# Kernel tuning notes

Measured on AMD Instinct MI355X. Metric: run time of the kernel, lower is better.

## Reference

```python
import jax, jax.numpy as jnp
import numpy as np

EPS = 1e-7  # same clamp torch BCE effectively applies to avoid log(0)


def _level_bce(att, boxes, valid, area, level_id, H, W):
    # att: [B, h_l, w_l] predicted attention in (0,1); boxes: [B, N, 4]; valid/area: [B, N]
    B, hl, wl = att.shape
    base = 2.0 ** (level_id + 5)
    min_area = base * base * 0.5
    max_area = (base * 1.58) ** 2 * 2.0
    sel = valid & (area >= min_area) & (area <= max_area)  # [B, N]
    sx = wl / W
    sy = hl / H
    # rasterization bounds on the level grid (int() == floor for non-negative coords)
    x1 = jnp.maximum(jnp.floor(boxes[..., 0] * sx), 0.0)
    y1 = jnp.maximum(jnp.floor(boxes[..., 1] * sy), 0.0)
    x2 = jnp.minimum(jnp.ceil(boxes[..., 2] * sx) + 1.0, float(wl))
    y2 = jnp.minimum(jnp.ceil(boxes[..., 3] * sy) + 1.0, float(hl))
    rows = jnp.arange(hl, dtype=att.dtype)
    cols = jnp.arange(wl, dtype=att.dtype)
    # separable per-box row/col indicators -> matmul-style OR to avoid a [B,N,h,w] tensor
    rin = (sel[..., None] & (rows >= y1[..., None]) & (rows < y2[..., None])).astype(att.dtype)  # [B,N,h]
    cin = (sel[..., None] & (cols >= x1[..., None]) & (cols < x2[..., None])).astype(att.dtype)  # [B,N,w]
    mask_gt = (jnp.einsum('bnh,bnw->bhw', rin, cin) > 0).astype(att.dtype)  # [B,h,w]
    p = jnp.clip(att, EPS, 1.0 - EPS)
    bce = -(mask_gt * jnp.log(p) + (1.0 - mask_gt) * jnp.log1p(-p))
    return bce.mean(axis=(1, 2))  # [B]


def reference(att0, att1, att2, att3, att4, bboxs, h, w):
    atts = [att0, att1, att2, att3, att4]
    hf = float(h)
    wf = float(w)
    x1, y1, x2, y2, label = (bboxs[..., i] for i in range(5))
    valid = (label != -1) & (x1 <= wf) & (y1 <= hf) & (x2 <= wf) & (y2 <= hf)  # [B,N]
    area = (x2 - x1) * (y2 - y1)
    boxes = bboxs[..., :4]
    per_level = [
        _level_bce(a[:, 0, :, :], boxes, valid, area, i, hf, wf)
        for i, a in enumerate(atts)
    ]
    sample_loss = jnp.stack(per_level, axis=0).mean(axis=0)  # [B]
    has_box = valid.any(axis=1)
    sample_loss = jnp.where(has_box, sample_loss, jnp.zeros_like(sample_loss))
    return sample_loss.mean(keepdims=True)  # [1]


def setup_inputs() -> dict:
    key = jax.random.key(0)
    ks = jax.random.split(key, 10)
    B, N, H, W = 16, 96, 4096, 4096
    sizes = [(1024, 1024), (512, 512), (256, 256), (128, 128), (64, 64)]
    inp = {}
    for i, (hl, wl) in enumerate(sizes):
        inp[f'att{i}'] = jax.random.uniform(ks[i], (B, 1, hl, wl), jnp.float32, 1e-4, 1.0 - 1e-4)
    cx = jax.random.uniform(ks[5], (B, N), jnp.float32) * W
    cy = jax.random.uniform(ks[6], (B, N), jnp.float32) * H
    side = jnp.exp(jax.random.uniform(ks[7], (B, N), jnp.float32, np.log(24.0), np.log(1100.0)))
    x1 = jnp.clip(cx - side / 2, 0.0, float(W))
    x2 = jnp.clip(cx + side / 2, 0.0, float(W))
    y1 = jnp.clip(cy - side / 2, 0.0, float(H))
    y2 = jnp.clip(cy + side / 2, 0.0, float(H))
    label = jnp.where(jax.random.uniform(ks[8], (B, N), jnp.float32) < 0.1, -1.0, 1.0)
    inp['bboxs'] = jnp.stack([x1, y1, x2, y2, label], axis=-1)
    inp['h'] = H
    inp['w'] = W
    return inp
```

## Files before the change

kernel.cpp:

```cpp
#include <hip/hip_runtime.h>

#define B_SZ 16
#define N_BOX 96
#define EPSF 1e-7f

#define MASK_BYTES 2793472u
#define ACC_STRIDE 32
#define ACC_BYTES  (B_SZ * 5 * ACC_STRIDE * 4)

__device__ __forceinline__ unsigned level_bit_off(int l) {
    switch (l) {
        case 0:  return 0u;
        case 1:  return 16777216u;
        case 2:  return 20971520u;
        case 3:  return 22020096u;
        default: return 22282240u;
    }
}

__global__ __launch_bounds__(64)
void raster_kernel(const float* __restrict__ bboxs,
                   const int* __restrict__ hp, const int* __restrict__ wp,
                   unsigned* __restrict__ maskbits)
{
    int gid = blockIdx.x;
    int n = gid % N_BOX;
    int l = (gid / N_BOX) % 5;
    int b = gid / (N_BOX * 5);

    const float* bx = bboxs + (b * N_BOX + n) * 5;
    float x1 = bx[0], y1 = bx[1], x2 = bx[2], y2 = bx[3], lb = bx[4];
    float Wf = (float)(*wp), Hf = (float)(*hp);

    bool valid = (lb != -1.0f) && (x1 <= Wf) && (y1 <= Hf) && (x2 <= Wf) && (y2 <= Hf);
    if (!valid) return;

    float area = (x2 - x1) * (y2 - y1);
    double based = (double)(32 << l);
    float mn  = (float)(based * based * 0.5);
    float mxv = (float)((based * 1.58) * (based * 1.58) * 2.0);
    if (!(area >= mn && area <= mxv)) return;

    int wl = 1024 >> l;
    float sx = (float)wl / Wf;
    float sy = (float)wl / Hf;

    int ix1 = (int)fmaxf(floorf(x1 * sx), 0.0f);
    int iy1 = (int)fmaxf(floorf(y1 * sy), 0.0f);
    int ix2 = (int)fminf(ceilf(x2 * sx) + 1.0f, (float)wl);
    int iy2 = (int)fminf(ceilf(y2 * sy) + 1.0f, (float)wl);
    if (ix2 <= ix1 || iy2 <= iy1) return;

    unsigned bitOff = level_bit_off(l) + (unsigned)b * (unsigned)(wl * wl);
    int nrows = iy2 - iy1;
    for (int rr = (int)threadIdx.x; rr < nrows; rr += 64) {
        int r = iy1 + rr;
        unsigned rs = bitOff + (unsigned)r * (unsigned)wl + (unsigned)ix1;
        unsigned re = rs + (unsigned)(ix2 - ix1);
        unsigned w0 = rs >> 5, w1 = (re - 1u) >> 5;
        for (unsigned w = w0; w <= w1; ++w) {
            unsigned lo = (w == w0) ? (rs & 31u) : 0u;
            unsigned hi = (w == w1) ? (((re - 1u) & 31u) + 1u) : 32u;
            unsigned m = (hi == 32u ? 0xffffffffu : ((1u << hi) - 1u)) & ~((1u << lo) - 1u);
            atomicOr(&maskbits[w], m);
        }
    }
}

__global__ __launch_bounds__(256)
void bce_kernel(const float* __restrict__ a0, const float* __restrict__ a1,
                const float* __restrict__ a2, const float* __restrict__ a3,
                const float* __restrict__ a4,
                const unsigned* __restrict__ maskbits,
                float* __restrict__ acc)
{
    int bid = blockIdx.x;
    int l, start, bppShift;
    const float* att;
    if (bid < 1024)      { l = 0; start = 0;    bppShift = 6; att = a0; }
    else if (bid < 1280) { l = 1; start = 1024; bppShift = 4; att = a1; }
    else if (bid < 1344) { l = 2; start = 1280; bppShift = 2; att = a2; }
    else if (bid < 1360) { l = 3; start = 1344; bppShift = 0; att = a3; }
    else                 { l = 4; start = 1360; bppShift = 0; att = a4; }

    int planeF4 = 1 << (18 - 2 * l);
    int bil = bid - start;
    int b     = bil >> bppShift;
    int chunk = bil & ((1 << bppShift) - 1);
    int nf4   = planeF4 >> bppShift;
    unsigned gf4base = (unsigned)b * (unsigned)planeF4 + (unsigned)(chunk * nf4);
    unsigned lvlBit  = level_bit_off(l);

    float s = 0.0f;
    for (int j0 = 0; j0 < nf4; j0 += 1024) {
        float4 av[4];
        unsigned nib[4];
        #pragma unroll
        for (int u = 0; u < 4; ++u) {
            unsigned gf4 = gf4base + (unsigned)(j0 + u * 256) + threadIdx.x;
            av[u] = reinterpret_cast<const float4*>(att)[gf4];
            unsigned bidx = lvlBit + gf4 * 4u;
            nib[u] = (maskbits[bidx >> 5] >> (bidx & 31u)) & 0xFu;
        }
        #pragma unroll
        for (int u = 0; u < 4; ++u) {
            float pv[4] = {av[u].x, av[u].y, av[u].z, av[u].w};
            #pragma unroll
            for (int j = 0; j < 4; ++j) {
                float p = fminf(fmaxf(pv[j], EPSF), 1.0f - EPSF);
                float q = ((nib[u] >> j) & 1u) ? p : (1.0f - p);
                s -= __logf(q);
            }
        }
    }

    #pragma unroll
    for (int off = 32; off > 0; off >>= 1)
        s += __shfl_down(s, off, 64);
    __shared__ float wsum[4];
    int lane = threadIdx.x & 63, wv = threadIdx.x >> 6;
    if (lane == 0) wsum[wv] = s;
    __syncthreads();
    if (threadIdx.x == 0) {
        float t = wsum[0] + wsum[1] + wsum[2] + wsum[3];
        atomicAdd(&acc[(b * 5 + l) * ACC_STRIDE], t);
    }
}

__global__ __launch_bounds__(256)
void finalize_kernel(const float* __restrict__ bboxs,
                     const int* __restrict__ hp, const int* __restrict__ wp,
                     const float* __restrict__ acc, float* __restrict__ out)
{
    __shared__ int hasbox[B_SZ];
    if (threadIdx.x < B_SZ) hasbox[threadIdx.x] = 0;
    __syncthreads();
    float Wf = (float)(*wp), Hf = (float)(*hp);
    for (int i = (int)threadIdx.x; i < B_SZ * N_BOX; i += 256) {
        const float* bx = bboxs + i * 5;
        if (bx[4] != -1.0f && bx[0] <= Wf && bx[1] <= Hf && bx[2] <= Wf && bx[3] <= Hf)
            hasbox[i / N_BOX] = 1;
    }
    __syncthreads();
    if (threadIdx.x == 0) {
        double tot = 0.0;
        for (int b = 0; b < B_SZ; ++b) {
            if (!hasbox[b]) continue;
            double s = 0.0;
            for (int l = 0; l < 5; ++l) {
                int wl = 1024 >> l;
                s += (double)acc[(b * 5 + l) * ACC_STRIDE] / (double)(wl * wl);
            }
            tot += s / 5.0;
        }
        out[0] = (float)(tot / (double)B_SZ);
    }
}

extern "C" void kernel_launch(void* const* d_in, const int* in_sizes, int n_in,
                              void* d_out, int out_size, void* d_ws, size_t ws_size,
                              hipStream_t stream)
{
    const float* a0 = (const float*)d_in[0];
    const float* a1 = (const float*)d_in[1];
    const float* a2 = (const float*)d_in[2];
    const float* a3 = (const float*)d_in[3];
    const float* a4 = (const float*)d_in[4];
    const float* bboxs = (const float*)d_in[5];
    const int* hp = (const int*)d_in[6];
    const int* wp = (const int*)d_in[7];

    unsigned* maskbits = (unsigned*)d_ws;
    float* acc = (float*)((char*)d_ws + MASK_BYTES);

    hipMemsetAsync(d_ws, 0, MASK_BYTES + ACC_BYTES, stream);
    raster_kernel<<<B_SZ * 5 * N_BOX, 64, 0, stream>>>(bboxs, hp, wp, maskbits);
    bce_kernel<<<1376, 256, 0, stream>>>(a0, a1, a2, a3, a4, maskbits, acc);
    finalize_kernel<<<1, 256, 0, stream>>>(bboxs, hp, wp, acc, (float*)d_out);
}
```

Measured before the change: 41.56 us.

## Double BCE grid with fixed per-block work and replace memset with clear kernel

New measurement: 41.47 us. Within noise of the previous version (-0.2%).

```diff
diff --git a/kernel.cpp b/kernel.cpp
--- a/kernel.cpp
+++ b/kernel.cpp
@@ -7,6 +7,7 @@
 #define MASK_BYTES 2793472u
 #define ACC_STRIDE 32
 #define ACC_BYTES  (B_SZ * 5 * ACC_STRIDE * 4)
+#define CLEAR_F4   ((MASK_BYTES + ACC_BYTES) / 16u)
 
 __device__ __forceinline__ unsigned level_bit_off(int l) {
     switch (l) {
@@ -16,6 +17,13 @@
         case 3:  return 22020096u;
         default: return 22282240u;
     }
+}
+
+__global__ __launch_bounds__(256)
+void clear_kernel(uint4* __restrict__ ws)
+{
+    unsigned i = blockIdx.x * 256u + threadIdx.x;
+    if (i < CLEAR_F4) ws[i] = make_uint4(0u, 0u, 0u, 0u);
 }
 
 __global__ __launch_bounds__(64)
@@ -77,27 +85,48 @@
     int bid = blockIdx.x;
     int l, start, bppShift;
     const float* att;
-    if (bid < 1024)      { l = 0; start = 0;    bppShift = 6; att = a0; }
-    else if (bid < 1280) { l = 1; start = 1024; bppShift = 4; att = a1; }
-    else if (bid < 1344) { l = 2; start = 1280; bppShift = 2; att = a2; }
-    else if (bid < 1360) { l = 3; start = 1344; bppShift = 0; att = a3; }
-    else                 { l = 4; start = 1360; bppShift = 0; att = a4; }
+    if (bid < 2048)      { l = 0; start = 0;    bppShift = 7; att = a0; }
+    else if (bid < 2560) { l = 1; start = 2048; bppShift = 5; att = a1; }
+    else if (bid < 2688) { l = 2; start = 2560; bppShift = 3; att = a2; }
+    else if (bid < 2720) { l = 3; start = 2688; bppShift = 1; att = a3; }
+    else                 { l = 4; start = 2720; bppShift = 0; att = a4; }
 
     int planeF4 = 1 << (18 - 2 * l);
     int bil = bid - start;
     int b     = bil >> bppShift;
     int chunk = bil & ((1 << bppShift) - 1);
     int nf4   = planeF4 >> bppShift;
-    unsigned gf4base = (unsigned)b * (unsigned)planeF4 + (unsigned)(chunk * nf4);
+    unsigned gf4base = (unsigned)b * (unsigned)planeF4
+                     + (unsigned)chunk * (unsigned)nf4 + threadIdx.x;
     unsigned lvlBit  = level_bit_off(l);
 
     float s = 0.0f;
-    for (int j0 = 0; j0 < nf4; j0 += 1024) {
+    if (nf4 == 2048) {
+        float4 av[8];
+        unsigned nib[8];
+        #pragma unroll
+        for (int u = 0; u < 8; ++u) {
+            unsigned gf4 = gf4base + (unsigned)(u * 256);
+            av[u] = reinterpret_cast<const float4*>(att)[gf4];
+            unsigned bidx = lvlBit + gf4 * 4u;
+            nib[u] = (maskbits[bidx >> 5] >> (bidx & 31u)) & 0xFu;
+        }
+        #pragma unroll
+        for (int u = 0; u < 8; ++u) {
+            float pv[4] = {av[u].x, av[u].y, av[u].z, av[u].w};
+            #pragma unroll
+            for (int j = 0; j < 4; ++j) {
+                float p = fminf(fmaxf(pv[j], EPSF), 1.0f - EPSF);
+                float q = ((nib[u] >> j) & 1u) ? p : (1.0f - p);
+                s -= __logf(q);
+            }
+        }
+    } else {
         float4 av[4];
         unsigned nib[4];
         #pragma unroll
         for (int u = 0; u < 4; ++u) {
-            unsigned gf4 = gf4base + (unsigned)(j0 + u * 256) + threadIdx.x;
+            unsigned gf4 = gf4base + (unsigned)(u * 256);
             av[u] = reinterpret_cast<const float4*>(att)[gf4];
             unsigned bidx = lvlBit + gf4 * 4u;
             nib[u] = (maskbits[bidx >> 5] >> (bidx & 31u)) & 0xFu;
@@ -173,8 +202,8 @@
     unsigned* maskbits = (unsigned*)d_ws;
     float* acc = (float*)((char*)d_ws + MASK_BYTES);
 
-    hipMemsetAsync(d_ws, 0, MASK_BYTES + ACC_BYTES, stream);
+    clear_kernel<<<(CLEAR_F4 + 255u) / 256u, 256, 0, stream>>>((uint4*)d_ws);
     raster_kernel<<<B_SZ * 5 * N_BOX, 64, 0, stream>>>(bboxs, hp, wp, maskbits);
-    bce_kernel<<<1376, 256, 0, stream>>>(a0, a1, a2, a3, a4, maskbits, acc);
+    bce_kernel<<<2736, 256, 0, stream>>>(a0, a1, a2, a3, a4, maskbits, acc);
     finalize_kernel<<<1, 256, 0, stream>>>(bboxs, hp, wp, acc, (float*)d_out);
 }
```
